# Kernel optimization log

Hardware: AMD Instinct MI355X
Metric: run time of the kernel (lower is better)

## Reference

```python
import jax, jax.numpy as jnp
import numpy as np

# Search geometry (matches init_kwargs)
WS, WT, PS, K, STRIDE0 = 9, 1, 7, 10, 4
SEARCH_INPUT = "noisy"
ALPHA = 0.5
CRIT = "l2"


def _extract_patches(vid, ti, hi, wi):
    """vid: [T,H,W,C]; ti/hi/wi int32 with shape [...] (patch top-left corners).
    Returns [..., PS*PS*C] with clamped (edge-replicated) boundary handling."""
    T, H, W, C = vid.shape
    dy = jnp.arange(PS)
    dx = jnp.arange(PS)
    hh = jnp.clip(hi[..., None, None] + dy[:, None], 0, H - 1)  # [...,PS,1]
    ww = jnp.clip(wi[..., None, None] + dx[None, :], 0, W - 1)  # [...,1,PS]
    p = vid[ti[..., None, None], hh, ww]  # [...,PS,PS,C]
    return p.reshape(p.shape[:-3] + (PS * PS * C,))


def _nls(vid, fflow, bflow):
    """NonLocalSearch: vid [T,H,W,C], flows [T,H,W,2] (channel 0 = x/w, 1 = y/h).
    Returns (topk_dists [nq,K], inds = (ti,hi,wi,tk,hk,wk))."""
    T, H, W, C = vid.shape
    nH, nW = H // STRIDE0, W // STRIDE0
    ti, hi, wi = jnp.meshgrid(jnp.arange(T), jnp.arange(nH) * STRIDE0,
                              jnp.arange(nW) * STRIDE0, indexing="ij")
    ti, hi, wi = ti.reshape(-1), hi.reshape(-1), wi.reshape(-1)  # [nq]
    q = _extract_patches(vid, ti, hi, wi)  # [nq, PS*PS*C]

    ff = fflow[ti, hi, wi]  # [nq,2] flow to frame t+1
    bf = bflow[ti, hi, wi]  # [nq,2] flow to frame t-1
    zero = jnp.zeros_like(ff)
    flow_dt = jnp.stack([bf, zero, ff], axis=1)  # [nq, 2*WT+1, 2] for dt=-1,0,+1
    dts = jnp.arange(-WT, WT + 1)
    tj = jnp.clip(ti[:, None] + dts[None, :], 0, T - 1)  # [nq, 2*WT+1]
    bh = jnp.clip(hi[:, None] + jnp.round(flow_dt[..., 1]).astype(jnp.int32), 0, H - 1)
    bw = jnp.clip(wi[:, None] + jnp.round(flow_dt[..., 0]).astype(jnp.int32), 0, W - 1)

    # Candidate schedule: (dt_index, oy, ox) for all (2*WT+1)*WS*WS candidates.
    r = WS // 2
    oy, ox = np.meshgrid(np.arange(-r, r + 1), np.arange(-r, r + 1), indexing="ij")
    nt = 2 * WT + 1
    specs = np.stack([np.repeat(np.arange(nt), WS * WS),
                      np.tile(oy.ravel(), nt),
                      np.tile(ox.ravel(), nt)], axis=1).astype(np.int32)  # [S,3]

    def step(_, spec):
        di, sy, sx = spec[0], spec[1], spec[2]
        tjc = tj[:, di]
        hj = jnp.clip(bh[:, di] + sy, 0, H - 1)
        wj = jnp.clip(bw[:, di] + sx, 0, W - 1)
        cp = _extract_patches(vid, tjc, hj, wj)  # [nq,D]
        d = jnp.sum((q - cp) ** 2, axis=-1)  # L2 patch distance, [nq]
        return None, (d, tjc, hj, wj)

    _, (dists, tjs, hjs, wjs) = jax.lax.scan(step, None, jnp.asarray(specs))
    # dists: [S, nq] -> top-K smallest per query
    negd, idx = jax.lax.top_k(-dists.T, K)  # [nq,K]
    tk = jnp.take_along_axis(tjs.T, idx, axis=1)
    hk = jnp.take_along_axis(hjs.T, idx, axis=1)
    wk = jnp.take_along_axis(wjs.T, idx, axis=1)
    return -negd, (ti, hi, wi, tk, hk, wk)


def _refine(vid, inds):
    """RefineSearch with wr=1,kr=1: recompute L2 patch distances at given inds."""
    ti, hi, wi, tk, hk, wk = inds
    q = _extract_patches(vid, ti, hi, wi)          # [nq, D]
    cp = _extract_patches(vid, tk, hk, wk)         # [nq, K, D]
    return jnp.sum((q[:, None, :] - cp) ** 2, axis=-1)  # [nq, K]


def setup_inputs() -> dict:
    key = jax.random.key(0)
    k1, k2, k3, k4 = jax.random.split(key, 4)
    B, T, C, H, W = 1, 5, 3, 384, 384
    noisy = jax.random.normal(k1, (B, T, C, H, W), dtype=jnp.float32)
    deno = jax.random.normal(k2, (B, T, C, H, W), dtype=jnp.float32)
    fflow = jax.random.normal(k3, (B, T, 2, H, W), dtype=jnp.float32)
    bflow = jax.random.normal(k4, (B, T, 2, H, W), dtype=jnp.float32)
    return {"noisy": noisy, "deno": deno, "fflow": fflow, "bflow": bflow}


def reference(noisy, deno, fflow, bflow):
    def per_video(nv, dv, ff, bf):
        nv_t = jnp.transpose(nv, (0, 2, 3, 1))  # [T,H,W,C]
        dv_t = jnp.transpose(dv, (0, 2, 3, 1))
        ff_t = jnp.transpose(ff, (0, 2, 3, 1))  # [T,H,W,2]
        bf_t = jnp.transpose(bf, (0, 2, 3, 1))
        if SEARCH_INPUT == "noisy":
            srch = nv_t
        elif SEARCH_INPUT == "deno":
            srch = dv_t
        else:  # interp
            srch = ALPHA * nv_t + (1.0 - ALPHA) * dv_t
        _, inds = _nls(srch, ff_t, bf_t)
        return _refine(nv_t, inds)  # [nq, K]

    dists = jax.vmap(per_video)(noisy, deno, fflow, bflow)  # [B, nq, K]
    if CRIT == "l1":
        return jnp.mean(jnp.sqrt(dists))
    return jnp.mean(dists)
```

## Files before the change

kernel.cpp:

```cpp
#include <hip/hip_runtime.h>

#define TT 5
#define HH 384
#define WW 384
#define CC 3
#define WSR 4
#define NH_ 96
#define NW_ 96
#define NQ_ (TT*NH_*NW_)
#define NCAND 243
#define KK 10

#define RROW 12
#define RSST 13

typedef _Float16 h2v __attribute__((ext_vector_type(2)));
union U32H2 { unsigned u; h2v h; };

static __device__ __forceinline__ unsigned pack_f16(float a, float b) {
    U32H2 u;
    u.h.x = (_Float16)a; u.h.y = (_Float16)b;
    return u.u;
}

static __device__ __forceinline__ unsigned wave_min63(unsigned x) {
    x = min(x, (unsigned)__builtin_amdgcn_update_dpp((int)x,(int)x,0x121,0xF,0xF,false));
    x = min(x, (unsigned)__builtin_amdgcn_update_dpp((int)x,(int)x,0x122,0xF,0xF,false));
    x = min(x, (unsigned)__builtin_amdgcn_update_dpp((int)x,(int)x,0x124,0xF,0xF,false));
    x = min(x, (unsigned)__builtin_amdgcn_update_dpp((int)x,(int)x,0x128,0xF,0xF,false));
    x = min(x, (unsigned)__builtin_amdgcn_update_dpp((int)x,(int)x,0x142,0xF,0xF,false));
    x = min(x, (unsigned)__builtin_amdgcn_update_dpp((int)x,(int)x,0x143,0xF,0xF,false));
    return x;
}

__global__ __launch_bounds__(256) void nls_kernel(
    const float* __restrict__ vid,
    const float* __restrict__ fflow,
    const float* __restrict__ bflow,
    float* __restrict__ ws)
{
    const int bid = blockIdx.x;
    const int q   = (bid & 7) * (NQ_/8) + (bid >> 3);
    const int tid = threadIdx.x;
    const int t   = q / (NH_*NW_);
    const int rem = q % (NH_*NW_);
    const int hi  = (rem / NW_) * 4;
    const int wi  = (rem % NW_) * 4;

    __shared__ alignas(16) unsigned reg_lds[135*RROW];
    __shared__ alignas(16) unsigned qp_lds[84];
    __shared__ alignas(16) float    rssd[189*RSST];
    __shared__ float dist[256];

    const float ffx = fflow[((t*2+0)*HH + hi)*WW + wi];
    const float ffy = fflow[((t*2+1)*HH + hi)*WW + wi];
    const float bfx = bflow[((t*2+0)*HH + hi)*WW + wi];
    const float bfy = bflow[((t*2+1)*HH + hi)*WW + wi];

    const int tj0 = max(t-1, 0);
    const int tj2 = min(t+1, TT-1);
    const int bh0 = min(max(hi + (int)rintf(bfy), 0), HH-1);
    const int bw0 = min(max(wi + (int)rintf(bfx), 0), WW-1);
    const int bh2 = min(max(hi + (int)rintf(ffy), 0), HH-1);
    const int bw2 = min(max(wi + (int)rintf(ffx), 0), WW-1);
    const int rm0 = max(bh0-WSR,0), rm1 = max(hi-WSR,0), rm2 = max(bh2-WSR,0);
    const int cm0 = max(bw0-WSR,0), cm1 = max(wi-WSR,0), cm2 = max(bw2-WSR,0);
    const int ca0 = cm0 & ~1,       ca1 = cm1 & ~1,      ca2 = cm2 & ~1;

    for (int i = tid; i < 270; i += 256) {
        int row = i >> 1, h = i & 1;
        int di  = row / 45; int r45 = row - di*45;
        int c   = r45 / 15; int r   = r45 - c*15;
        int tjd = (di==0)?tj0:((di==1)?t  :tj2);
        int rm  = (di==0)?rm0:((di==1)?rm1:rm2);
        int ca  = (di==0)?ca0:((di==1)?ca1:ca2);
        int rr  = min(rm + r, HH-1);
        const float* vrow = vid + (size_t)((tjd*CC+c)*HH + rr)*WW;
        int c0 = ca + 8*h;
        float f0,f1,f2,f3,f4,f5,f6,f7;
        if (ca <= 368) {
            float2 p0 = *(const float2*)(vrow + c0);
            float2 p1 = *(const float2*)(vrow + c0 + 2);
            float2 p2 = *(const float2*)(vrow + c0 + 4);
            float2 p3 = *(const float2*)(vrow + c0 + 6);
            f0=p0.x; f1=p0.y; f2=p1.x; f3=p1.y; f4=p2.x; f5=p2.y; f6=p3.x; f7=p3.y;
        } else {
            f0=vrow[min(c0,  WW-1)]; f1=vrow[min(c0+1,WW-1)];
            f2=vrow[min(c0+2,WW-1)]; f3=vrow[min(c0+3,WW-1)];
            f4=vrow[min(c0+4,WW-1)]; f5=vrow[min(c0+5,WW-1)];
            f6=vrow[min(c0+6,WW-1)]; f7=vrow[min(c0+7,WW-1)];
        }
        uint4 w;
        w.x = pack_f16(f0,f1); w.y = pack_f16(f2,f3);
        w.z = pack_f16(f4,f5); w.w = pack_f16(f6,f7);
        *(uint4*)&reg_lds[row*RROW + 4*h] = w;
    }
    if (tid < 84) {
        int c  = tid / 28;
        int rr = tid - c*28;
        int dy = rr >> 2;
        int k  = rr & 3;
        int row = min(hi+dy, HH-1);
        const float* vrow = vid + (size_t)((t*CC + c)*HH + row)*WW;
        float v0 = vrow[min(wi + 2*k, WW-1)];
        float v1 = (k==3) ? 0.0f : vrow[min(wi + 2*k + 1, WW-1)];
        qp_lds[tid] = pack_f16(v0, v1);
    }
    __syncthreads();

    if (tid < 189) {
        int di   = tid / 63; int r63 = tid - di*63;
        int roff = r63 / 7;  int dy  = r63 - roff*7;
        int rr   = roff + dy;
        float rs[10];
        #pragma unroll
        for (int w = 0; w < 10; w++) rs[w] = 0.f;
        #pragma unroll
        for (int c = 0; c < 3; c++) {
            int base = ((di*3 + c)*15 + rr)*RROW;
            uint4 va0 = *(const uint4*)&reg_lds[base];
            uint4 va1 = *(const uint4*)&reg_lds[base + 4];
            uint4 vq  = *(const uint4*)&qp_lds[c*28 + dy*4];
            unsigned A[8], B[8];
            A[0]=va0.x; A[1]=va0.y; A[2]=va0.z; A[3]=va0.w;
            A[4]=va1.x; A[5]=va1.y; A[6]=va1.z; A[7]=va1.w;
            #pragma unroll
            for (int j = 0; j < 7; j++) B[j] = (A[j] >> 16) | (A[j+1] << 16);
            B[7] = A[7] >> 16;
            U32H2 q0,q1,q2,q3;
            q0.u = vq.x; q1.u = vq.y; q2.u = vq.z; q3.u = vq.w;
            #pragma unroll
            for (int w = 0; w < 10; w++) {
                const int off = w >> 1;
                U32H2 c0,c1,c2,c3;
                if (w & 1) { c0.u=B[off]; c1.u=B[off+1]; c2.u=B[off+2]; c3.u=B[off+3]; }
                else       { c0.u=A[off]; c1.u=A[off+1]; c2.u=A[off+2]; c3.u=A[off+3]; }
                U32H2 d0,d1,d2,d3;
                d0.h = c0.h - q0.h;
                d1.h = c1.h - q1.h;
                d2.h = c2.h - q2.h;
                d3.h = c3.h - q3.h;
                d3.u &= 0x0000FFFFu;
                float s = rs[w];
                s = __builtin_amdgcn_fdot2(d0.h, d0.h, s, false);
                s = __builtin_amdgcn_fdot2(d1.h, d1.h, s, false);
                s = __builtin_amdgcn_fdot2(d2.h, d2.h, s, false);
                s = __builtin_amdgcn_fdot2(d3.h, d3.h, s, false);
                rs[w] = s;
            }
        }
        int ob = tid * RSST;
        #pragma unroll
        for (int w = 0; w < 10; w++) rssd[ob + w] = rs[w];
    }
    __syncthreads();

    float dmy = __int_as_float(0x7f800000);
    if (tid < NCAND) {
        int di  = tid / 81; int s81 = tid - di*81;
        int syq = s81 / 9;  int sx  = s81 - syq*9 - WSR;
        int sy  = syq - WSR;
        int bhd = (di==0)?bh0:((di==1)?hi :bh2);
        int bwd = (di==0)?bw0:((di==1)?wi :bw2);
        int rm  = (di==0)?rm0:((di==1)?rm1:rm2);
        int ca  = (di==0)?ca0:((di==1)?ca1:ca2);
        int hj = min(max(bhd + sy, 0), HH-1);
        int wj = min(max(bwd + sx, 0), WW-1);
        int roff = hj - rm;
        int wof  = wj - ca;
        int ib = (di*63 + roff*7)*RSST + wof;
        float s = 0.f;
        #pragma unroll
        for (int dy = 0; dy < 7; dy++) s += rssd[ib + dy*RSST];
        dmy = s;
    }
    dist[tid] = dmy;
    __syncthreads();

    if (tid < 64) {
        unsigned k0 = (__float_as_uint(dist[tid    ]) & 0xFFFFFF00u) | (unsigned)tid;
        unsigned k1 = (__float_as_uint(dist[tid+ 64]) & 0xFFFFFF00u) | (unsigned)(tid+64);
        unsigned k2 = (__float_as_uint(dist[tid+128]) & 0xFFFFFF00u) | (unsigned)(tid+128);
        unsigned k3 = (__float_as_uint(dist[tid+192]) & 0xFFFFFF00u) | (unsigned)(tid+192);
        float sumk = 0.f;
        #pragma unroll 1
        for (int k = 0; k < KK; k++) {
            unsigned loc = min(min(k0,k1), min(k2,k3));
            unsigned wm  = wave_min63(loc);
            unsigned m   = (unsigned)__builtin_amdgcn_readlane((int)wm, 63);
            sumk += __uint_as_float(m & 0xFFFFFF00u);
            int slot = (int)(m & 0xFFu);
            k0 = (slot == (int)tid      ) ? 0xFFFFFFFFu : k0;
            k1 = (slot == (int)tid + 64 ) ? 0xFFFFFFFFu : k1;
            k2 = (slot == (int)tid + 128) ? 0xFFFFFFFFu : k2;
            k3 = (slot == (int)tid + 192) ? 0xFFFFFFFFu : k3;
        }
        if (tid == 0) ws[q] = sumk;
    }
}

__global__ __launch_bounds__(256) void reduce1_kernel(
    const float* __restrict__ ws, float* __restrict__ out)
{
    float s = ws[blockIdx.x*256 + threadIdx.x];
    #pragma unroll
    for (int o = 32; o > 0; o >>= 1) s += __shfl_down(s, o, 64);
    __shared__ float sd[4];
    int w = threadIdx.x >> 6, l = threadIdx.x & 63;
    if (l == 0) sd[w] = s;
    __syncthreads();
    if (threadIdx.x == 0) {
        float tot = sd[0] + sd[1] + sd[2] + sd[3];
        atomicAdd(out, tot * (1.0f / ((float)NQ_ * (float)KK)));
    }
}

extern "C" void kernel_launch(void* const* d_in, const int* in_sizes, int n_in,
                              void* d_out, int out_size, void* d_ws, size_t ws_size,
                              hipStream_t stream) {
    const float* noisy = (const float*)d_in[0];
    const float* fflow = (const float*)d_in[2];
    const float* bflow = (const float*)d_in[3];
    float* ws  = (float*)d_ws;
    float* out = (float*)d_out;

    hipMemsetAsync(out, 0, sizeof(float), stream);
    nls_kernel<<<NQ_, 256, 0, stream>>>(noisy, fflow, bflow, ws);
    reduce1_kernel<<<NQ_/256, 256, 0, stream>>>(ws, out);
}
```

Measured before the change: 269.0 us.

## Shrink NLS kernel to single-wave blocks processing time offsets sequentially

Each query block now runs as one 64-lane wavefront instead of 256 threads. The three temporal offsets are processed in a loop that reuses a smaller row-SSD buffer, and the candidate keys go straight into registers for the wave-level top-k, so the dist LDS array and its extra barrier are gone. This aims to cut idle threads, LDS footprint and block-wide sync cost, so more blocks can fit per CU. In exchange, each wave does three times more serial work per query, and the unpadded stride-10 rssd layout may cause LDS bank conflicts.

```diff
diff --git a/kernel.cpp b/kernel.cpp
--- a/kernel.cpp
+++ b/kernel.cpp
@@ -12,7 +12,6 @@
 #define KK 10
 
 #define RROW 12
-#define RSST 13
 
 typedef _Float16 h2v __attribute__((ext_vector_type(2)));
 union U32H2 { unsigned u; h2v h; };
@@ -33,24 +32,23 @@
     return x;
 }
 
-__global__ __launch_bounds__(256) void nls_kernel(
+__global__ __launch_bounds__(64, 4) void nls_kernel(
     const float* __restrict__ vid,
     const float* __restrict__ fflow,
     const float* __restrict__ bflow,
     float* __restrict__ ws)
 {
-    const int bid = blockIdx.x;
-    const int q   = (bid & 7) * (NQ_/8) + (bid >> 3);
-    const int tid = threadIdx.x;
-    const int t   = q / (NH_*NW_);
-    const int rem = q % (NH_*NW_);
-    const int hi  = (rem / NW_) * 4;
-    const int wi  = (rem % NW_) * 4;
+    const int bid  = blockIdx.x;
+    const int q    = (bid & 7) * (NQ_/8) + (bid >> 3);
+    const int lane = threadIdx.x;
+    const int t    = q / (NH_*NW_);
+    const int rem  = q % (NH_*NW_);
+    const int hi   = (rem / NW_) * 4;
+    const int wi   = (rem % NW_) * 4;
 
     __shared__ alignas(16) unsigned reg_lds[135*RROW];
     __shared__ alignas(16) unsigned qp_lds[84];
-    __shared__ alignas(16) float    rssd[189*RSST];
-    __shared__ float dist[256];
+    __shared__ float rssd[630];
 
     const float ffx = fflow[((t*2+0)*HH + hi)*WW + wi];
     const float ffy = fflow[((t*2+1)*HH + hi)*WW + wi];
@@ -67,7 +65,7 @@
     const int cm0 = max(bw0-WSR,0), cm1 = max(wi-WSR,0), cm2 = max(bw2-WSR,0);
     const int ca0 = cm0 & ~1,       ca1 = cm1 & ~1,      ca2 = cm2 & ~1;
 
-    for (int i = tid; i < 270; i += 256) {
+    for (int i = lane; i < 270; i += 64) {
         int row = i >> 1, h = i & 1;
         int di  = row / 45; int r45 = row - di*45;
         int c   = r45 / 15; int r   = r45 - c*15;
@@ -95,93 +93,99 @@
         w.z = pack_f16(f4,f5); w.w = pack_f16(f6,f7);
         *(uint4*)&reg_lds[row*RROW + 4*h] = w;
     }
-    if (tid < 84) {
-        int c  = tid / 28;
-        int rr = tid - c*28;
+    for (int i = lane; i < 84; i += 64) {
+        int c  = i / 28;
+        int rr = i - c*28;
         int dy = rr >> 2;
         int k  = rr & 3;
         int row = min(hi+dy, HH-1);
         const float* vrow = vid + (size_t)((t*CC + c)*HH + row)*WW;
         float v0 = vrow[min(wi + 2*k, WW-1)];
         float v1 = (k==3) ? 0.0f : vrow[min(wi + 2*k + 1, WW-1)];
-        qp_lds[tid] = pack_f16(v0, v1);
+        qp_lds[i] = pack_f16(v0, v1);
     }
     __syncthreads();
 
-    if (tid < 189) {
-        int di   = tid / 63; int r63 = tid - di*63;
-        int roff = r63 / 7;  int dy  = r63 - roff*7;
-        int rr   = roff + dy;
-        float rs[10];
+    unsigned k0 = 0xFFFFFFFFu, k1 = 0xFFFFFFFFu, k2 = 0xFFFFFFFFu, k3 = 0xFFFFFFFFu;
+
+    for (int di = 0; di < 3; ++di) {
+        if (lane < 63) {
+            int roff = lane / 7, dy = lane - roff*7;
+            int rr   = roff + dy;
+            float rs[10];
+            #pragma unroll
+            for (int w = 0; w < 10; w++) rs[w] = 0.f;
+            #pragma unroll
+            for (int c = 0; c < 3; c++) {
+                int base = ((di*3 + c)*15 + rr)*RROW;
+                uint4 va0 = *(const uint4*)&reg_lds[base];
+                uint4 va1 = *(const uint4*)&reg_lds[base + 4];
+                uint4 vq  = *(const uint4*)&qp_lds[c*28 + dy*4];
+                unsigned A[8], B[8];
+                A[0]=va0.x; A[1]=va0.y; A[2]=va0.z; A[3]=va0.w;
+                A[4]=va1.x; A[5]=va1.y; A[6]=va1.z; A[7]=va1.w;
+                #pragma unroll
+                for (int j = 0; j < 7; j++) B[j] = (A[j] >> 16) | (A[j+1] << 16);
+                B[7] = A[7] >> 16;
+                U32H2 q0,q1,q2,q3;
+                q0.u = vq.x; q1.u = vq.y; q2.u = vq.z; q3.u = vq.w;
+                #pragma unroll
+                for (int w = 0; w < 10; w++) {
+                    const int off = w >> 1;
+                    U32H2 c0,c1,c2,c3;
+                    if (w & 1) { c0.u=B[off]; c1.u=B[off+1]; c2.u=B[off+2]; c3.u=B[off+3]; }
+                    else       { c0.u=A[off]; c1.u=A[off+1]; c2.u=A[off+2]; c3.u=A[off+3]; }
+                    U32H2 d0,d1,d2,d3;
+                    d0.h = c0.h - q0.h;
+                    d1.h = c1.h - q1.h;
+                    d2.h = c2.h - q2.h;
+                    d3.h = c3.h - q3.h;
+                    d3.u &= 0x0000FFFFu;
+                    float s = rs[w];
+                    s = __builtin_amdgcn_fdot2(d0.h, d0.h, s, false);
+                    s = __builtin_amdgcn_fdot2(d1.h, d1.h, s, false);
+                    s = __builtin_amdgcn_fdot2(d2.h, d2.h, s, false);
+                    s = __builtin_amdgcn_fdot2(d3.h, d3.h, s, false);
+                    rs[w] = s;
+                }
+            }
+            int ob = lane * 10;
+            #pragma unroll
+            for (int w = 0; w < 10; w++) rssd[ob + w] = rs[w];
+        }
+        __syncthreads();
+
+        const int bhd = (di==0)?bh0:((di==1)?hi :bh2);
+        const int bwd = (di==0)?bw0:((di==1)?wi :bw2);
+        const int rm  = (di==0)?rm0:((di==1)?rm1:rm2);
+        const int ca  = (di==0)?ca0:((di==1)?ca1:ca2);
         #pragma unroll
-        for (int w = 0; w < 10; w++) rs[w] = 0.f;
-        #pragma unroll
-        for (int c = 0; c < 3; c++) {
-            int base = ((di*3 + c)*15 + rr)*RROW;
-            uint4 va0 = *(const uint4*)&reg_lds[base];
-            uint4 va1 = *(const uint4*)&reg_lds[base + 4];
-            uint4 vq  = *(const uint4*)&qp_lds[c*28 + dy*4];
-            unsigned A[8], B[8];
-            A[0]=va0.x; A[1]=va0.y; A[2]=va0.z; A[3]=va0.w;
-            A[4]=va1.x; A[5]=va1.y; A[6]=va1.z; A[7]=va1.w;
-            #pragma unroll
-            for (int j = 0; j < 7; j++) B[j] = (A[j] >> 16) | (A[j+1] << 16);
-            B[7] = A[7] >> 16;
-            U32H2 q0,q1,q2,q3;
-            q0.u = vq.x; q1.u = vq.y; q2.u = vq.z; q3.u = vq.w;
-            #pragma unroll
-            for (int w = 0; w < 10; w++) {
-                const int off = w >> 1;
-                U32H2 c0,c1,c2,c3;
-                if (w & 1) { c0.u=B[off]; c1.u=B[off+1]; c2.u=B[off+2]; c3.u=B[off+3]; }
-                else       { c0.u=A[off]; c1.u=A[off+1]; c2.u=A[off+2]; c3.u=A[off+3]; }
-                U32H2 d0,d1,d2,d3;
-                d0.h = c0.h - q0.h;
-                d1.h = c1.h - q1.h;
-                d2.h = c2.h - q2.h;
-                d3.h = c3.h - q3.h;
-                d3.u &= 0x0000FFFFu;
-                float s = rs[w];
-                s = __builtin_amdgcn_fdot2(d0.h, d0.h, s, false);
-                s = __builtin_amdgcn_fdot2(d1.h, d1.h, s, false);
-                s = __builtin_amdgcn_fdot2(d2.h, d2.h, s, false);
-                s = __builtin_amdgcn_fdot2(d3.h, d3.h, s, false);
-                rs[w] = s;
+        for (int j = 0; j < 4; j++) {
+            int c   = j*64 + lane;
+            int s81 = c - di*81;
+            if (s81 >= 0 && s81 < 81) {
+                int syq = s81 / 9;
+                int sx  = s81 - syq*9 - WSR;
+                int sy  = syq - WSR;
+                int hj = min(max(bhd + sy, 0), HH-1);
+                int wj = min(max(bwd + sx, 0), WW-1);
+                int roff = hj - rm;
+                int wof  = wj - ca;
+                int ib = roff*70 + wof;
+                float s = 0.f;
+                #pragma unroll
+                for (int dy = 0; dy < 7; dy++) s += rssd[ib + dy*10];
+                unsigned key = (__float_as_uint(s) & 0xFFFFFF00u) | (unsigned)c;
+                if (j==0) k0 = key;
+                if (j==1) k1 = key;
+                if (j==2) k2 = key;
+                if (j==3) k3 = key;
             }
         }
-        int ob = tid * RSST;
-        #pragma unroll
-        for (int w = 0; w < 10; w++) rssd[ob + w] = rs[w];
-    }
-    __syncthreads();
-
-    float dmy = __int_as_float(0x7f800000);
-    if (tid < NCAND) {
-        int di  = tid / 81; int s81 = tid - di*81;
-        int syq = s81 / 9;  int sx  = s81 - syq*9 - WSR;
-        int sy  = syq - WSR;
-        int bhd = (di==0)?bh0:((di==1)?hi :bh2);
-        int bwd = (di==0)?bw0:((di==1)?wi :bw2);
-        int rm  = (di==0)?rm0:((di==1)?rm1:rm2);
-        int ca  = (di==0)?ca0:((di==1)?ca1:ca2);
-        int hj = min(max(bhd + sy, 0), HH-1);
-        int wj = min(max(bwd + sx, 0), WW-1);
-        int roff = hj - rm;
-        int wof  = wj - ca;
-        int ib = (di*63 + roff*7)*RSST + wof;
-        float s = 0.f;
-        #pragma unroll
-        for (int dy = 0; dy < 7; dy++) s += rssd[ib + dy*RSST];
-        dmy = s;
-    }
-    dist[tid] = dmy;
-    __syncthreads();
-
-    if (tid < 64) {
-        unsigned k0 = (__float_as_uint(dist[tid    ]) & 0xFFFFFF00u) | (unsigned)tid;
-        unsigned k1 = (__float_as_uint(dist[tid+ 64]) & 0xFFFFFF00u) | (unsigned)(tid+64);
-        unsigned k2 = (__float_as_uint(dist[tid+128]) & 0xFFFFFF00u) | (unsigned)(tid+128);
-        unsigned k3 = (__float_as_uint(dist[tid+192]) & 0xFFFFFF00u) | (unsigned)(tid+192);
+        __syncthreads();
+    }
+
+    {
         float sumk = 0.f;
         #pragma unroll 1
         for (int k = 0; k < KK; k++) {
@@ -190,12 +194,12 @@
             unsigned m   = (unsigned)__builtin_amdgcn_readlane((int)wm, 63);
             sumk += __uint_as_float(m & 0xFFFFFF00u);
             int slot = (int)(m & 0xFFu);
-            k0 = (slot == (int)tid      ) ? 0xFFFFFFFFu : k0;
-            k1 = (slot == (int)tid + 64 ) ? 0xFFFFFFFFu : k1;
-            k2 = (slot == (int)tid + 128) ? 0xFFFFFFFFu : k2;
-            k3 = (slot == (int)tid + 192) ? 0xFFFFFFFFu : k3;
-        }
-        if (tid == 0) ws[q] = sumk;
+            k0 = (slot == lane      ) ? 0xFFFFFFFFu : k0;
+            k1 = (slot == lane + 64 ) ? 0xFFFFFFFFu : k1;
+            k2 = (slot == lane + 128) ? 0xFFFFFFFFu : k2;
+            k3 = (slot == lane + 192) ? 0xFFFFFFFFu : k3;
+        }
+        if (lane == 0) ws[q] = sumk;
     }
 }
 
@@ -225,6 +229,6 @@
     float* out = (float*)d_out;
 
     hipMemsetAsync(out, 0, sizeof(float), stream);
-    nls_kernel<<<NQ_, 256, 0, stream>>>(noisy, fflow, bflow, ws);
+    nls_kernel<<<NQ_, 64, 0, stream>>>(noisy, fflow, bflow, ws);
     reduce1_kernel<<<NQ_/256, 256, 0, stream>>>(ws, out);
 }
```

New measurement: 269.8 us. No clear change (+0.3%).
